# Kernel optimization log

Measured on AMD Instinct MI355X. Metric: run time of the kernel, lower is better.

## Reference

```python
import jax, jax.numpy as jnp
import numpy as np

B, N, C, H = 8, 1024, 768, 12
HD = C // H
SCALE = HD ** -0.5


def setup_inputs() -> dict:
    key = jax.random.key(0)
    k1, k2, k3 = jax.random.split(key, 3)
    x = jax.random.normal(k1, (B, N, C), dtype=jnp.float32)
    # parameter init roughly matching nn.Linear default scale
    w_qkv = jax.random.normal(k2, (C, 3 * C), dtype=jnp.float32) * (C ** -0.5)
    w_out = jax.random.normal(k3, (C, C), dtype=jnp.float32) * (C ** -0.5)
    b_out = jnp.zeros((C,), dtype=jnp.float32)
    return {"x": x, "w_qkv": w_qkv, "w_out": w_out, "b_out": b_out}


def reference(x, w_qkv, w_out, b_out):
    b, n, c = x.shape
    qkv = x @ w_qkv                                   # [b, n, 3c]
    q, k, v = jnp.split(qkv, 3, axis=-1)
    # [b, n, c] -> [b, heads, n, head_dim]
    def to_heads(t):
        return t.reshape(b, n, H, HD).transpose(0, 2, 1, 3)
    q, k, v = to_heads(q), to_heads(k), to_heads(v)
    dots = jnp.einsum('bhqd,bhkd->bhqk', q, k) * SCALE  # [b, h, n, n]
    attn = jax.nn.softmax(dots, axis=-1)
    # dropout is identity in eval mode
    out = jnp.einsum('bhqk,bhkd->bhqd', attn, v)        # [b, h, n, hd]
    out = out.transpose(0, 2, 1, 3).reshape(b, n, c)
    return out @ w_out + b_out
```

## Files before the change

### kernel.cpp

```cpp
#include <hip/hip_runtime.h>
#include <stdint.h>


typedef __attribute__((ext_vector_type(8))) __bf16 bf16x8;
typedef __attribute__((ext_vector_type(4))) float f32x4;

__device__ __forceinline__ uint16_t f2bf(float f) {
    union { float f; unsigned u; } c; c.f = f;
    unsigned x = c.u;
    unsigned r = (x + 0x7FFFu + ((x >> 16) & 1u)) >> 16;
    return (uint16_t)r;
}

__device__ __forceinline__ void gload_lds16(const uint16_t* g, uint16_t* l) {
    __builtin_amdgcn_global_load_lds(
        (const __attribute__((address_space(1))) unsigned int*)g,
        (__attribute__((address_space(3))) unsigned int*)l, 16, 0, 0);
}

__global__ __launch_bounds__(256) void prep(
    const float* __restrict__ x, uint16_t* __restrict__ xbf,
    const float* __restrict__ w_qkv, uint16_t* __restrict__ wtqkv,
    const float* __restrict__ w_out, uint16_t* __restrict__ wtout) {
    __shared__ uint16_t tile[32][33];
    int bid = blockIdx.x;
    int tid = threadIdx.x;

    if (bid < 3072) {
        int i = (bid * 256 + tid) * 8;
        float4 a = *(const float4*)(x + i);
        float4 b = *(const float4*)(x + i + 4);
        union { uint16_t u[8]; uint4 v; } o;
        o.u[0] = f2bf(a.x); o.u[1] = f2bf(a.y); o.u[2] = f2bf(a.z); o.u[3] = f2bf(a.w);
        o.u[4] = f2bf(b.x); o.u[5] = f2bf(b.y); o.u[6] = f2bf(b.z); o.u[7] = f2bf(b.w);
        *(uint4*)(xbf + i) = o.v;
        return;
    }

    const float* src; uint16_t* dst; int Cc, bx, by;
    if (bid < 4800) {
        int id = bid - 3072;
        src = w_qkv; dst = wtqkv; Cc = 2304;
        bx = id % 72; by = id / 72;
    } else {
        int id = bid - 4800;
        src = w_out; dst = wtout; Cc = 768;
        bx = id % 24; by = id / 24;
    }
    const int R = 768;
    int tx = tid & 31, ty = tid >> 5;
    int c0 = bx * 32, r0 = by * 32;
#pragma unroll
    for (int i = 0; i < 4; i++) {
        int r = ty + i * 8;
        tile[r][tx] = f2bf(src[(size_t)(r0 + r) * Cc + c0 + tx]);
    }
    __syncthreads();
#pragma unroll
    for (int i = 0; i < 4; i++) {
        int r = ty + i * 8;
        dst[(size_t)(c0 + r) * R + r0 + tx] = tile[tx][r];
    }
}

template <int MODE>
__global__ __launch_bounds__(256) void gemm128(
    const uint16_t* __restrict__ A, const uint16_t* __restrict__ Bt,
    int Kdim, int Ncols,
    uint16_t* __restrict__ qws, uint16_t* __restrict__ kws,
    uint16_t* __restrict__ vtws,
    const float* __restrict__ bias, float* __restrict__ outp) {
    __shared__ uint16_t lA[2][2][2048];
    __shared__ uint16_t lB[2][2][4096];

    int tid = threadIdx.x;
    int w = tid >> 6, lane = tid & 63, quad = lane >> 4, lo = lane & 15;
    int mw = w >> 1, nw = w & 1;

    int nwg = gridDim.x * gridDim.y;
    int lid = blockIdx.y * gridDim.x + blockIdx.x;
    int swzid = (lid & 7) * (nwg >> 3) + (lid >> 3);
    int m0 = (swzid / gridDim.x) * 64;
    int n0 = (swzid % gridDim.x) * 128;

    int srow = tid >> 2;
    int skc = ((tid & 3) ^ ((tid >> 3) & 3)) * 8;
    const uint16_t* gA0 = A + (size_t)(m0 + srow) * Kdim + skc;
    const uint16_t* gB0 = Bt + (size_t)(n0 + srow) * Kdim + skc;
    const uint16_t* gB1 = gB0 + (size_t)64 * Kdim;

    f32x4 acc[2][4];
#pragma unroll
    for (int i = 0; i < 2; i++)
#pragma unroll
        for (int j = 0; j < 4; j++) acc[i][j] = (f32x4){0.f, 0.f, 0.f, 0.f};

    int swz = (quad ^ ((lo >> 1) & 3)) * 8;
    int aoff = (mw * 32 + lo) * 32 + swz;
    int boff = (nw * 64 + lo) * 32 + swz;

    const int nIter = Kdim >> 6;

#pragma unroll
    for (int s = 0; s < 2; s++) {
        gload_lds16(gA0 + s * 32, &lA[0][s][tid * 8]);
        gload_lds16(gB0 + s * 32, &lB[0][s][tid * 8]);
        gload_lds16(gB1 + s * 32, &lB[0][s][2048 + tid * 8]);
    }
    __syncthreads();

    for (int it = 0; it < nIter; it++) {
        const int cur = it & 1, nxt = cur ^ 1;
        const int kn = (it + 1 < nIter) ? (it + 1) * 64 : 0;

#pragma unroll
        for (int s = 0; s < 2; s++) {
            gload_lds16(gA0 + kn + s * 32, &lA[nxt][s][tid * 8]);
            gload_lds16(gB0 + kn + s * 32, &lB[nxt][s][tid * 8]);
            gload_lds16(gB1 + kn + s * 32, &lB[nxt][s][2048 + tid * 8]);
        }

#pragma unroll
        for (int s = 0; s < 2; s++) {
            bf16x8 af[2], bfr[4];
#pragma unroll
            for (int i = 0; i < 2; i++) af[i] = *(const bf16x8*)(&lA[cur][s][aoff + i * 512]);
#pragma unroll
            for (int j = 0; j < 4; j++) bfr[j] = *(const bf16x8*)(&lB[cur][s][boff + j * 512]);
#pragma unroll
            for (int i = 0; i < 2; i++)
#pragma unroll
                for (int j = 0; j < 4; j++)
                    acc[i][j] = __builtin_amdgcn_mfma_f32_16x16x32_bf16(
                        af[i], bfr[j], acc[i][j], 0, 0, 0);
        }
        __syncthreads();
    }

    if (MODE == 0) {
        int part = n0 / 768;
        int ccb = n0 % 768 + nw * 64;
        float qsc = (part == 0) ? 0.18033688011112042f : 1.0f;
#pragma unroll
        for (int i = 0; i < 2; i++)
#pragma unroll
            for (int j = 0; j < 4; j++)
#pragma unroll
                for (int r = 0; r < 4; r++) {
                    int m = m0 + mw * 32 + i * 16 + quad * 4 + r;
                    int bidx = m >> 10, nidx = m & 1023;
                    int cc = ccb + j * 16 + lo;
                    int h = cc >> 6, d = cc & 63;
                    int bh = bidx * 12 + h;
                    uint16_t v = f2bf(acc[i][j][r] * qsc);
                    int kt = nidx >> 5, keyin = nidx & 31;
                    if (part == 0) {
                        qws[((size_t)bh * 1024 + nidx) * 64 + d] = v;
                    } else if (part == 1) {
                        int fs = ((d >> 5) << 1) | (keyin & 1);
                        int idx = ((bh << 5) + kt) * 2048 + fs * 512 +
                                  ((((d & 31) >> 3) << 4) + (keyin >> 1)) * 8 + (d & 7);
                        kws[idx] = v;
                    } else {
                        int idx = ((bh << 5) + kt) * 2048 + (d >> 4) * 512 +
                                  (((keyin >> 3) << 4) + (d & 15)) * 8 + (keyin & 7);
                        vtws[idx] = v;
                    }
                }
    } else {
#pragma unroll
        for (int i = 0; i < 2; i++)
#pragma unroll
            for (int j = 0; j < 4; j++)
#pragma unroll
                for (int r = 0; r < 4; r++) {
                    int m = m0 + mw * 32 + i * 16 + quad * 4 + r;
                    int c = n0 + nw * 64 + j * 16 + lo;
                    outp[(size_t)m * Ncols + c] = acc[i][j][r] + bias[c];
                }
    }
}

__global__ __launch_bounds__(256) void attn_kernel(
    const uint16_t* __restrict__ qws, const uint16_t* __restrict__ kws,
    const uint16_t* __restrict__ vtws, uint16_t* __restrict__ attnout) {
    int bh = blockIdx.x;
    int qt = blockIdx.y;
    int tid = threadIdx.x;
    int w = tid >> 6, lane = tid & 63, quad = lane >> 4, lo = lane & 15;
    int q0 = qt * 128 + w * 32;

    const uint16_t* Qb = qws + (size_t)bh * 65536;
    const uint16_t* Kt = kws + (size_t)bh * 65536;
    const uint16_t* Vt = vtws + (size_t)bh * 65536;

    bf16x8 aq[2][2];
#pragma unroll
    for (int rg = 0; rg < 2; rg++)
#pragma unroll
        for (int h = 0; h < 2; h++)
            aq[rg][h] = *(const bf16x8*)(Qb + (size_t)(q0 + rg * 16 + lo) * 64 + h * 32 + quad * 8);

    f32x4 oacc[2][4], ol[2];
#pragma unroll
    for (int rg = 0; rg < 2; rg++) {
        ol[rg] = (f32x4){0.f, 0.f, 0.f, 0.f};
#pragma unroll
        for (int nd = 0; nd < 4; nd++) oacc[rg][nd] = (f32x4){0.f, 0.f, 0.f, 0.f};
    }

    bf16x8 ones;
#pragma unroll
    for (int i = 0; i < 8; i++) ones[i] = (__bf16)1.0f;

    __shared__ uint16_t P[4][2][16][40];

    const f32x4 zero4 = (f32x4){0.f, 0.f, 0.f, 0.f};

#pragma unroll 2
    for (int kt = 0; kt < 32; kt++) {
        const uint16_t* Kb = Kt + kt * 2048;
        const uint16_t* Vb = Vt + kt * 2048;

        bf16x8 bk[2][2], vv[4];
#pragma unroll
        for (int t = 0; t < 2; t++)
#pragma unroll
            for (int h = 0; h < 2; h++)
                bk[t][h] = *(const bf16x8*)(Kb + (h * 2 + t) * 512 + lane * 8);
#pragma unroll
        for (int nd = 0; nd < 4; nd++)
            vv[nd] = *(const bf16x8*)(Vb + nd * 512 + lane * 8);

#pragma unroll
        for (int rg = 0; rg < 2; rg++) {
            f32x4 s0 = __builtin_amdgcn_mfma_f32_16x16x32_bf16(aq[rg][0], bk[0][0], zero4, 0, 0, 0);
            s0 = __builtin_amdgcn_mfma_f32_16x16x32_bf16(aq[rg][1], bk[0][1], s0, 0, 0, 0);
            f32x4 s1 = __builtin_amdgcn_mfma_f32_16x16x32_bf16(aq[rg][0], bk[1][0], zero4, 0, 0, 0);
            s1 = __builtin_amdgcn_mfma_f32_16x16x32_bf16(aq[rg][1], bk[1][1], s1, 0, 0, 0);
#pragma unroll
            for (int r = 0; r < 4; r++) {
                union { float f; unsigned u; } u0, u1;
                u0.f = __builtin_exp2f(s0[r]);
                u1.f = __builtin_exp2f(s1[r]);
                unsigned pk = __builtin_amdgcn_perm(u1.u, u0.u, 0x07060302u);
                *(unsigned*)&P[w][rg][quad * 4 + r][2 * lo] = pk;
            }
        }

#pragma unroll
        for (int rg = 0; rg < 2; rg++) {
            bf16x8 ap = *(const bf16x8*)(&P[w][rg][lo][quad * 8]);
            ol[rg] = __builtin_amdgcn_mfma_f32_16x16x32_bf16(ap, ones, ol[rg], 0, 0, 0);
#pragma unroll
            for (int nd = 0; nd < 4; nd++)
                oacc[rg][nd] = __builtin_amdgcn_mfma_f32_16x16x32_bf16(ap, vv[nd], oacc[rg][nd], 0, 0, 0);
        }
    }

    int b = bh / 12, hh = bh % 12;
#pragma unroll
    for (int rg = 0; rg < 2; rg++)
#pragma unroll
        for (int r = 0; r < 4; r++) {
            float inv = 1.0f / ol[rg][r];
            int n = q0 + rg * 16 + quad * 4 + r;
            size_t base = ((size_t)(b * 1024 + n)) * 768 + hh * 64;
#pragma unroll
            for (int nd = 0; nd < 4; nd++)
                attnout[base + nd * 16 + lo] = f2bf(oacc[rg][nd][r] * inv);
        }
}

extern "C" void kernel_launch(void* const* d_in, const int* in_sizes, int n_in,
                              void* d_out, int out_size, void* d_ws, size_t ws_size,
                              hipStream_t stream) {
    const float* x     = (const float*)d_in[0];
    const float* w_qkv = (const float*)d_in[1];
    const float* w_out = (const float*)d_in[2];
    const float* b_out = (const float*)d_in[3];
    float* out = (float*)d_out;

    char* ws = (char*)d_ws;
    uint16_t* xbf   = (uint16_t*)(ws);
    uint16_t* qws   = (uint16_t*)(ws + 12582912);
    uint16_t* kws   = (uint16_t*)(ws + 25165824);
    uint16_t* vtws  = (uint16_t*)(ws + 37748736);
    uint16_t* attn  = (uint16_t*)(ws + 50331648);
    uint16_t* wtqkv = (uint16_t*)(ws + 62914560);
    uint16_t* wtout = (uint16_t*)(ws + 66453504);

    prep<<<5376, 256, 0, stream>>>(x, xbf, w_qkv, wtqkv, w_out, wtout);

    gemm128<0><<<dim3(18, 128), 256, 0, stream>>>(
        xbf, wtqkv, 768, 2304, qws, kws, vtws, nullptr, nullptr);

    attn_kernel<<<dim3(96, 8), 256, 0, stream>>>(qws, kws, vtws, attn);

    gemm128<1><<<dim3(6, 128), 256, 0, stream>>>(
        attn, wtout, 768, 768, nullptr, nullptr, nullptr, b_out, out);
}
```

Measured before the change: 198.8 us.

## Fuse all stages into one persistent kernel with grid barriers

Replaces the four separate launches (prep, QKV GEMM, attention, output GEMM) with a single persistent kernel of 768 blocks. Each block loops over work units of each stage, and stages are separated by atomic-counter grid barriers. Shared memory is unioned across the stages. This removes inter-kernel launch gaps, but relies on all 768 blocks being co-resident (launch bounds of 3 blocks per CU). It also drops the L2-friendly block swizzle in the GEMMs and adds a memset plus barrier spin cost.

```diff
diff --git a/kernel.cpp b/kernel.cpp
--- a/kernel.cpp
+++ b/kernel.cpp
@@ -18,14 +18,29 @@
         (__attribute__((address_space(3))) unsigned int*)l, 16, 0, 0);
 }
 
-__global__ __launch_bounds__(256) void prep(
-    const float* __restrict__ x, uint16_t* __restrict__ xbf,
+__device__ __forceinline__ void grid_barrier(unsigned* bar) {
+    __threadfence();
+    __syncthreads();
+    if (threadIdx.x == 0) {
+        __hip_atomic_fetch_add(bar, 1u, __ATOMIC_RELEASE, __HIP_MEMORY_SCOPE_AGENT);
+        while (__hip_atomic_load(bar, __ATOMIC_RELAXED, __HIP_MEMORY_SCOPE_AGENT) < 768u)
+            __builtin_amdgcn_s_sleep(16);
+        (void)__hip_atomic_load(bar, __ATOMIC_ACQUIRE, __HIP_MEMORY_SCOPE_AGENT);
+    }
+    __syncthreads();
+}
+
+union SMem {
+    struct { uint16_t lA[2 * 2 * 2048]; uint16_t lB[2 * 2 * 4096]; } g;
+    uint16_t P[4 * 2 * 16 * 40];
+    uint16_t tile[32][33];
+};
+
+__device__ __forceinline__ void prep_unit(
+    int bid, int tid, const float* __restrict__ x, uint16_t* __restrict__ xbf,
     const float* __restrict__ w_qkv, uint16_t* __restrict__ wtqkv,
-    const float* __restrict__ w_out, uint16_t* __restrict__ wtout) {
-    __shared__ uint16_t tile[32][33];
-    int bid = blockIdx.x;
-    int tid = threadIdx.x;
-
+    const float* __restrict__ w_out, uint16_t* __restrict__ wtout,
+    uint16_t (*tile)[33]) {
     if (bid < 3072) {
         int i = (bid * 256 + tid) * 8;
         float4 a = *(const float4*)(x + i);
@@ -34,54 +49,46 @@
         o.u[0] = f2bf(a.x); o.u[1] = f2bf(a.y); o.u[2] = f2bf(a.z); o.u[3] = f2bf(a.w);
         o.u[4] = f2bf(b.x); o.u[5] = f2bf(b.y); o.u[6] = f2bf(b.z); o.u[7] = f2bf(b.w);
         *(uint4*)(xbf + i) = o.v;
-        return;
-    }
-
-    const float* src; uint16_t* dst; int Cc, bx, by;
-    if (bid < 4800) {
-        int id = bid - 3072;
-        src = w_qkv; dst = wtqkv; Cc = 2304;
-        bx = id % 72; by = id / 72;
     } else {
-        int id = bid - 4800;
-        src = w_out; dst = wtout; Cc = 768;
-        bx = id % 24; by = id / 24;
-    }
-    const int R = 768;
-    int tx = tid & 31, ty = tid >> 5;
-    int c0 = bx * 32, r0 = by * 32;
-#pragma unroll
-    for (int i = 0; i < 4; i++) {
-        int r = ty + i * 8;
-        tile[r][tx] = f2bf(src[(size_t)(r0 + r) * Cc + c0 + tx]);
-    }
-    __syncthreads();
-#pragma unroll
-    for (int i = 0; i < 4; i++) {
-        int r = ty + i * 8;
-        dst[(size_t)(c0 + r) * R + r0 + tx] = tile[tx][r];
+        const float* src; uint16_t* dst; int Cc, bx, by;
+        if (bid < 4800) {
+            int id = bid - 3072;
+            src = w_qkv; dst = wtqkv; Cc = 2304;
+            bx = id % 72; by = id / 72;
+        } else {
+            int id = bid - 4800;
+            src = w_out; dst = wtout; Cc = 768;
+            bx = id % 24; by = id / 24;
+        }
+        const int R = 768;
+        int tx = tid & 31, ty = tid >> 5;
+        int c0 = bx * 32, r0 = by * 32;
+#pragma unroll
+        for (int i = 0; i < 4; i++) {
+            int r = ty + i * 8;
+            tile[r][tx] = f2bf(src[(size_t)(r0 + r) * Cc + c0 + tx]);
+        }
+        __syncthreads();
+#pragma unroll
+        for (int i = 0; i < 4; i++) {
+            int r = ty + i * 8;
+            dst[(size_t)(c0 + r) * R + r0 + tx] = tile[tx][r];
+        }
+        __syncthreads();
     }
 }
 
 template <int MODE>
-__global__ __launch_bounds__(256) void gemm128(
-    const uint16_t* __restrict__ A, const uint16_t* __restrict__ Bt,
-    int Kdim, int Ncols,
+__device__ __forceinline__ void gemm_tile(
+    int bx, int by, const uint16_t* __restrict__ A, const uint16_t* __restrict__ Bt,
+    int Kdim, int Ncols, uint16_t* lA, uint16_t* lB,
     uint16_t* __restrict__ qws, uint16_t* __restrict__ kws,
     uint16_t* __restrict__ vtws,
     const float* __restrict__ bias, float* __restrict__ outp) {
-    __shared__ uint16_t lA[2][2][2048];
-    __shared__ uint16_t lB[2][2][4096];
-
     int tid = threadIdx.x;
     int w = tid >> 6, lane = tid & 63, quad = lane >> 4, lo = lane & 15;
     int mw = w >> 1, nw = w & 1;
-
-    int nwg = gridDim.x * gridDim.y;
-    int lid = blockIdx.y * gridDim.x + blockIdx.x;
-    int swzid = (lid & 7) * (nwg >> 3) + (lid >> 3);
-    int m0 = (swzid / gridDim.x) * 64;
-    int n0 = (swzid % gridDim.x) * 128;
+    int m0 = by * 64, n0 = bx * 128;
 
     int srow = tid >> 2;
     int skc = ((tid & 3) ^ ((tid >> 3) & 3)) * 8;
@@ -103,9 +110,9 @@
 
 #pragma unroll
     for (int s = 0; s < 2; s++) {
-        gload_lds16(gA0 + s * 32, &lA[0][s][tid * 8]);
-        gload_lds16(gB0 + s * 32, &lB[0][s][tid * 8]);
-        gload_lds16(gB1 + s * 32, &lB[0][s][2048 + tid * 8]);
+        gload_lds16(gA0 + s * 32, lA + s * 2048 + tid * 8);
+        gload_lds16(gB0 + s * 32, lB + s * 4096 + tid * 8);
+        gload_lds16(gB1 + s * 32, lB + s * 4096 + 2048 + tid * 8);
     }
     __syncthreads();
 
@@ -115,18 +122,20 @@
 
 #pragma unroll
         for (int s = 0; s < 2; s++) {
-            gload_lds16(gA0 + kn + s * 32, &lA[nxt][s][tid * 8]);
-            gload_lds16(gB0 + kn + s * 32, &lB[nxt][s][tid * 8]);
-            gload_lds16(gB1 + kn + s * 32, &lB[nxt][s][2048 + tid * 8]);
+            gload_lds16(gA0 + kn + s * 32, lA + (nxt * 2 + s) * 2048 + tid * 8);
+            gload_lds16(gB0 + kn + s * 32, lB + (nxt * 2 + s) * 4096 + tid * 8);
+            gload_lds16(gB1 + kn + s * 32, lB + (nxt * 2 + s) * 4096 + 2048 + tid * 8);
         }
 
 #pragma unroll
         for (int s = 0; s < 2; s++) {
             bf16x8 af[2], bfr[4];
 #pragma unroll
-            for (int i = 0; i < 2; i++) af[i] = *(const bf16x8*)(&lA[cur][s][aoff + i * 512]);
-#pragma unroll
-            for (int j = 0; j < 4; j++) bfr[j] = *(const bf16x8*)(&lB[cur][s][boff + j * 512]);
+            for (int i = 0; i < 2; i++)
+                af[i] = *(const bf16x8*)(lA + (cur * 2 + s) * 2048 + aoff + i * 512);
+#pragma unroll
+            for (int j = 0; j < 4; j++)
+                bfr[j] = *(const bf16x8*)(lB + (cur * 2 + s) * 4096 + boff + j * 512);
 #pragma unroll
             for (int i = 0; i < 2; i++)
 #pragma unroll
@@ -181,11 +190,10 @@
     }
 }
 
-__global__ __launch_bounds__(256) void attn_kernel(
-    const uint16_t* __restrict__ qws, const uint16_t* __restrict__ kws,
-    const uint16_t* __restrict__ vtws, uint16_t* __restrict__ attnout) {
-    int bh = blockIdx.x;
-    int qt = blockIdx.y;
+__device__ __forceinline__ void attn_tile(
+    int bh, int qt, const uint16_t* __restrict__ qws,
+    const uint16_t* __restrict__ kws, const uint16_t* __restrict__ vtws,
+    uint16_t* __restrict__ attnout, uint16_t* Pb) {
     int tid = threadIdx.x;
     int w = tid >> 6, lane = tid & 63, quad = lane >> 4, lo = lane & 15;
     int q0 = qt * 128 + w * 32;
@@ -212,8 +220,6 @@
     bf16x8 ones;
 #pragma unroll
     for (int i = 0; i < 8; i++) ones[i] = (__bf16)1.0f;
-
-    __shared__ uint16_t P[4][2][16][40];
 
     const f32x4 zero4 = (f32x4){0.f, 0.f, 0.f, 0.f};
 
@@ -244,13 +250,13 @@
                 u0.f = __builtin_exp2f(s0[r]);
                 u1.f = __builtin_exp2f(s1[r]);
                 unsigned pk = __builtin_amdgcn_perm(u1.u, u0.u, 0x07060302u);
-                *(unsigned*)&P[w][rg][quad * 4 + r][2 * lo] = pk;
+                *(unsigned*)(Pb + ((w * 2 + rg) * 16 + quad * 4 + r) * 40 + 2 * lo) = pk;
             }
         }
 
 #pragma unroll
         for (int rg = 0; rg < 2; rg++) {
-            bf16x8 ap = *(const bf16x8*)(&P[w][rg][lo][quad * 8]);
+            bf16x8 ap = *(const bf16x8*)(Pb + ((w * 2 + rg) * 16 + lo) * 40 + quad * 8);
             ol[rg] = __builtin_amdgcn_mfma_f32_16x16x32_bf16(ap, ones, ol[rg], 0, 0, 0);
 #pragma unroll
             for (int nd = 0; nd < 4; nd++)
@@ -270,6 +276,39 @@
             for (int nd = 0; nd < 4; nd++)
                 attnout[base + nd * 16 + lo] = f2bf(oacc[rg][nd][r] * inv);
         }
+}
+
+__global__ __launch_bounds__(256, 3) void mega(
+    const float* __restrict__ x, const float* __restrict__ w_qkv,
+    const float* __restrict__ w_out, const float* __restrict__ b_out,
+    uint16_t* __restrict__ xbf, uint16_t* __restrict__ qws,
+    uint16_t* __restrict__ kws, uint16_t* __restrict__ vtws,
+    uint16_t* __restrict__ attnws, uint16_t* __restrict__ wtqkv,
+    uint16_t* __restrict__ wtout, float* __restrict__ outp,
+    unsigned* bar) {
+    __shared__ SMem sm;
+    int bx = blockIdx.x, tid = threadIdx.x;
+
+    for (int r = 0; r < 7; r++)
+        prep_unit(r * 768 + bx, tid, x, xbf, w_qkv, wtqkv, w_out, wtout,
+                  (uint16_t(*)[33])sm.tile);
+
+    grid_barrier(bar + 0);
+
+    for (int r = 0; r < 3; r++) {
+        int v = r * 768 + bx;
+        gemm_tile<0>(v % 18, v / 18, xbf, wtqkv, 768, 2304, sm.g.lA, sm.g.lB,
+                     qws, kws, vtws, nullptr, nullptr);
+    }
+
+    grid_barrier(bar + 1);
+
+    attn_tile(bx % 96, bx / 96, qws, kws, vtws, attnws, sm.P);
+
+    grid_barrier(bar + 2);
+
+    gemm_tile<1>(bx % 6, bx / 6, attnws, wtout, 768, 768, sm.g.lA, sm.g.lB,
+                 nullptr, nullptr, nullptr, b_out, outp);
 }
 
 extern "C" void kernel_launch(void* const* d_in, const int* in_sizes, int n_in,
@@ -282,21 +321,18 @@
     float* out = (float*)d_out;
 
     char* ws = (char*)d_ws;
-    uint16_t* xbf   = (uint16_t*)(ws);
-    uint16_t* qws   = (uint16_t*)(ws + 12582912);
-    uint16_t* kws   = (uint16_t*)(ws + 25165824);
-    uint16_t* vtws  = (uint16_t*)(ws + 37748736);
-    uint16_t* attn  = (uint16_t*)(ws + 50331648);
-    uint16_t* wtqkv = (uint16_t*)(ws + 62914560);
-    uint16_t* wtout = (uint16_t*)(ws + 66453504);
-
-    prep<<<5376, 256, 0, stream>>>(x, xbf, w_qkv, wtqkv, w_out, wtout);
-
-    gemm128<0><<<dim3(18, 128), 256, 0, stream>>>(
-        xbf, wtqkv, 768, 2304, qws, kws, vtws, nullptr, nullptr);
-
-    attn_kernel<<<dim3(96, 8), 256, 0, stream>>>(qws, kws, vtws, attn);
-
-    gemm128<1><<<dim3(6, 128), 256, 0, stream>>>(
-        attn, wtout, 768, 768, nullptr, nullptr, nullptr, b_out, out);
-}
+    const size_t OFF = 4096;
+    unsigned* bar   = (unsigned*)ws;
+    uint16_t* xbf   = (uint16_t*)(ws + OFF);
+    uint16_t* qws   = (uint16_t*)(ws + OFF + 12582912);
+    uint16_t* kws   = (uint16_t*)(ws + OFF + 25165824);
+    uint16_t* vtws  = (uint16_t*)(ws + OFF + 37748736);
+    uint16_t* attn  = (uint16_t*)(ws + OFF + 50331648);
+    uint16_t* wtqkv = (uint16_t*)(ws + OFF + 62914560);
+    uint16_t* wtout = (uint16_t*)(ws + OFF + 66453504);
+
+    hipMemsetAsync(ws, 0, 64, stream);
+
+    mega<<<768, 256, 0, stream>>>(x, w_qkv, w_out, b_out, xbf, qws, kws, vtws,
+                                  attn, wtqkv, wtout, out, bar);
+}
```

After: 628.8 us. 3.16x slower.
